# Kernel tuning notes

Measured on AMD Instinct MI355X. Metric: run time of the kernel, lower is better.

The kernel has to match this reference:

```python
import jax, jax.numpy as jnp
import numpy as np


def _apply_1q_batched(state, gate, q):
    # state: (B,2,2,2,2) complex; gate: (B,2,2) complex; acts on qubit q
    state = jnp.moveaxis(state, q + 1, -1)
    state = jnp.einsum('bij,b...j->b...i', gate, state)
    return jnp.moveaxis(state, -1, q + 1)


def _apply_cnot(state, c, t):
    # flip target bit where control bit == 1
    s0, s1 = jnp.split(state, 2, axis=c + 1)
    s1 = jnp.flip(s1, axis=t + 1)
    return jnp.concatenate([s0, s1], axis=c + 1)


def _quantum_features(angles, params):
    # angles: (B,4) RY rotation angles; params: (4,) RZ angles
    B = angles.shape[0]
    state = jnp.zeros((B, 16), jnp.complex64).at[:, 0].set(1.0).reshape(B, 2, 2, 2, 2)
    # RY(x_i) on each wire (batched angle per sample)
    for q in range(4):
        th = 0.5 * angles[:, q]
        c, s = jnp.cos(th), jnp.sin(th)
        gate = jnp.stack([jnp.stack([c, -s], -1), jnp.stack([s, c], -1)], -2).astype(jnp.complex64)
        state = _apply_1q_batched(state, gate, q)
    # RZ(params[i]) on wire i followed by CNOT(i, (i+1)%4), interleaved as in source
    pc = params.astype(jnp.complex64)
    for q in range(4):
        ph = jnp.exp(jnp.array([-0.5j, 0.5j], jnp.complex64) * pc[q])
        shp = [1, 1, 1, 1, 1]
        shp[q + 1] = 2
        state = state * ph.reshape(shp)
        state = _apply_cnot(state, q, (q + 1) % 4)
    probs = state.real ** 2 + state.imag ** 2  # (B,2,2,2,2)
    feats = []
    for q in range(4):
        axes = tuple(a for a in range(1, 5) if a != q + 1)
        p = probs.sum(axes)  # (B,2)
        feats.append(p[:, 0] - p[:, 1])  # <Z_q>
    return jnp.stack(feats, -1)  # (B,4)


def _deconv2x2(x, w, b):
    # PyTorch ConvTranspose2d with kernel=stride=2, padding=0 (non-overlapping)
    # x: (B,Ci,H,W), w: (Ci,Co,2,2), b: (Co,)
    B, Ci, H, W = x.shape
    Co = w.shape[1]
    y = jnp.einsum('bchw,codk->bohdwk', x, w).reshape(B, Co, 2 * H, 2 * W)
    return y + b[None, :, None, None]


def setup_inputs() -> dict:
    key = jax.random.key(0)
    ks = jax.random.split(key, 10)
    B = 16384
    return {
        'x': jax.random.uniform(ks[0], (B, 1, 28, 28), jnp.float32),
        'var_params': jax.random.normal(ks[1], (4,), jnp.float32),
        'w_lat': jax.random.normal(ks[2], (224, 4), jnp.float32) * 0.3,
        'b_lat': jax.random.normal(ks[3], (224,), jnp.float32) * 0.05,
        'w_fc': jax.random.normal(ks[4], (392, 224), jnp.float32) * 0.05,
        'b_fc': jax.random.normal(ks[5], (392,), jnp.float32) * 0.05,
        'w_d1': jax.random.normal(ks[6], (8, 4, 2, 2), jnp.float32) * 0.2,
        'b_d1': jax.random.normal(ks[7], (4,), jnp.float32) * 0.05,
        'w_d2': jax.random.normal(ks[8], (4, 1, 2, 2), jnp.float32) * 0.2,
        'b_d2': jax.random.normal(ks[9], (1,), jnp.float32) * 0.05,
    }


def reference(x, var_params, w_lat, b_lat, w_fc, b_fc, w_d1, b_d1, w_d2, b_d2):
    # quadrant means -> 4 angles per sample
    quad = jnp.stack([
        x[:, 0, :14, :14].mean((1, 2)),
        x[:, 0, :14, 14:].mean((1, 2)),
        x[:, 0, 14:, :14].mean((1, 2)),
        x[:, 0, 14:, 14:].mean((1, 2)),
    ], axis=1)  # (B,4)
    qf = _quantum_features(quad, var_params)  # (B,4)
    latent = jax.nn.relu(qf @ w_lat.T + b_lat)  # (B,224)
    h = jax.nn.relu(latent @ w_fc.T + b_fc)  # (B,392)
    h = h.reshape(-1, 8, 7, 7)
    h = jax.nn.relu(_deconv2x2(h, w_d1, b_d1))  # (B,4,14,14)
    out = jax.nn.sigmoid(_deconv2x2(h, w_d2, b_d2))  # (B,1,28,28)
    return out
```

## Files before the change

kernel.cpp:

```cpp
#include <hip/hip_runtime.h>
#include <math.h>

#define G 16
#define HS 396
#define LSTR 232

typedef __attribute__((ext_vector_type(8))) __bf16 bf16x8;
typedef __attribute__((ext_vector_type(4))) float f32x4;

__global__ void wconv_kernel(const float* __restrict__ w_fc, __bf16* __restrict__ wb) {
  int tile = blockIdx.x;
  int kt   = blockIdx.y;
  int lane = threadIdx.x;
  int n  = tile * 16 + (lane & 15);
  int k0 = kt * 32 + (lane >> 4) * 8;
  bf16x8 v;
  if (n < 392) {
    const float* src = w_fc + (size_t)n * 224 + k0;
    float4 f0 = *(const float4*)(src);
    float4 f1 = *(const float4*)(src + 4);
    v[0] = (__bf16)f0.x; v[1] = (__bf16)f0.y; v[2] = (__bf16)f0.z; v[3] = (__bf16)f0.w;
    v[4] = (__bf16)f1.x; v[5] = (__bf16)f1.y; v[6] = (__bf16)f1.z; v[7] = (__bf16)f1.w;
  } else {
    #pragma unroll
    for (int j = 0; j < 8; ++j) v[j] = (__bf16)0.f;
  }
  *(bf16x8*)(wb + ((size_t)(tile * 7 + kt) * 64 + lane) * 8) = v;
}

__global__ __launch_bounds__(256) void qsum_kernel(
    const float* __restrict__ x, float* __restrict__ angles, int B)
{
  int wave = threadIdx.x >> 6;
  int lane = threadIdx.x & 63;
  int s = blockIdx.x * 4 + wave;
  if (s >= B) return;
  const float4* xs4 = (const float4*)(x + (size_t)s * 784);
  float st0 = 0.f, st1 = 0.f, sb0 = 0.f, sb1 = 0.f;
  for (int i4 = lane; i4 < 196; i4 += 64) {
    float4 v = xs4[i4];
    int base = i4 * 4;
    int r = base / 28;
    int cb = base - r * 28;
    float bt = (r >= 14) ? 1.f : 0.f;
    float tp = 1.f - bt;
    float vals[4] = {v.x, v.y, v.z, v.w};
    #pragma unroll
    for (int e = 0; e < 4; ++e) {
      float val = vals[e];
      bool right = (cb + e) >= 14;
      float l = right ? 0.f : val;
      float rr = right ? val : 0.f;
      st0 = fmaf(tp, l, st0);
      st1 = fmaf(tp, rr, st1);
      sb0 = fmaf(bt, l, sb0);
      sb1 = fmaf(bt, rr, sb1);
    }
  }
  #pragma unroll
  for (int o = 32; o > 0; o >>= 1) {
    st0 += __shfl_down(st0, o, 64);
    st1 += __shfl_down(st1, o, 64);
    sb0 += __shfl_down(sb0, o, 64);
    sb1 += __shfl_down(sb1, o, 64);
  }
  if (lane == 0) {
    const float inv = 1.f / 196.f;
    float4 o;
    o.x = st0 * inv; o.y = st1 * inv; o.z = sb0 * inv; o.w = sb1 * inv;
    *(float4*)(angles + 4 * s) = o;
  }
}

__global__ __launch_bounds__(256) void qsim_kernel(
    const float* __restrict__ params, float* __restrict__ qfa, int B)
{
  int s = blockIdx.x * 256 + threadIdx.x;
  if (s >= B) return;
  float4 mn = *(const float4*)(qfa + 4 * s);
  float means[4] = {mn.x, mn.y, mn.z, mn.w};
  float cs[4], sn[4];
  #pragma unroll
  for (int q = 0; q < 4; ++q) {
    float th = 0.5f * means[q];
    sn[q] = __sinf(th);
    cs[q] = __cosf(th);
  }
  float re[16], im[16];
  #pragma unroll
  for (int idx = 0; idx < 16; ++idx) {
    float a = ((idx >> 3) & 1) ? sn[0] : cs[0];
    a *= ((idx >> 2) & 1) ? sn[1] : cs[1];
    a *= ((idx >> 1) & 1) ? sn[2] : cs[2];
    a *= (idx & 1) ? sn[3] : cs[3];
    re[idx] = a;
    im[idx] = 0.f;
  }
  #pragma unroll
  for (int q = 0; q < 4; ++q) {
    float hp = 0.5f * params[q];
    float sp = __sinf(hp), cp = __cosf(hp);
    int qb = 3 - q;
    #pragma unroll
    for (int idx = 0; idx < 16; ++idx) {
      float sg = ((idx >> qb) & 1) ? sp : -sp;
      float r0 = re[idx], i0 = im[idx];
      re[idx] = r0 * cp - i0 * sg;
      im[idx] = r0 * sg + i0 * cp;
    }
    int cm = 1 << qb;
    int tm = 1 << (3 - ((q + 1) & 3));
    #pragma unroll
    for (int idx = 0; idx < 16; ++idx) {
      if ((idx & cm) && !(idx & tm)) {
        int j = idx | tm;
        float tr = re[idx]; re[idx] = re[j]; re[j] = tr;
        float ti = im[idx]; im[idx] = im[j]; im[j] = ti;
      }
    }
  }
  float z[4];
  #pragma unroll
  for (int q = 0; q < 4; ++q) {
    int qb = 3 - q;
    float acc = 0.f;
    #pragma unroll
    for (int idx = 0; idx < 16; ++idx) {
      float p = re[idx] * re[idx] + im[idx] * im[idx];
      acc += ((idx >> qb) & 1) ? -p : p;
    }
    z[q] = acc;
  }
  float4 o; o.x = z[0]; o.y = z[1]; o.z = z[2]; o.w = z[3];
  *(float4*)(qfa + 4 * s) = o;
}

__global__ __launch_bounds__(256) void decoder_kernel(
    const float* __restrict__ qf, const __bf16* __restrict__ wb,
    const float* __restrict__ w_lat, const float* __restrict__ b_lat,
    const float* __restrict__ b_fc,
    const float* __restrict__ w_d1, const float* __restrict__ b_d1,
    const float* __restrict__ w_d2, const float* __restrict__ b_d2,
    float* __restrict__ out, int B)
{
  __shared__ __align__(16) __bf16 latb[G * LSTR];
  __shared__ __align__(16) float hbuf[G * HS];
  __shared__ float qfs[G * 4];
  __shared__ float wd1[128];
  __shared__ float wd2[16];
  __shared__ float bd1[4];
  const int t = threadIdx.x;
  const int s0g = blockIdx.x * G;

  if (t < 64) qfs[t] = qf[s0g * 4 + t];
  else if (t < 192) wd1[t - 64] = w_d1[t - 64];
  else if (t < 208) wd2[t - 192] = w_d2[t - 192];
  else if (t < 212) bd1[t - 208] = b_d1[t - 208];
  __syncthreads();

  for (int v = t; v < G * 224; v += 256) {
    int s = v / 224;
    int j = v - s * 224;
    float4 w = *(const float4*)(w_lat + j * 4);
    float a = b_lat[j];
    a = fmaf(qfs[s * 4 + 0], w.x, a);
    a = fmaf(qfs[s * 4 + 1], w.y, a);
    a = fmaf(qfs[s * 4 + 2], w.z, a);
    a = fmaf(qfs[s * 4 + 3], w.w, a);
    latb[s * LSTR + j] = (__bf16)fmaxf(a, 0.f);
  }
  __syncthreads();

  {
    const int wv = t >> 6;
    const int lane = t & 63;
    const int m = lane & 15;
    const int kq = lane >> 4;
    const __bf16* arow = latb + m * LSTR + kq * 8;
    for (int tile = wv; tile < 25; tile += 4) {
      f32x4 acc = {0.f, 0.f, 0.f, 0.f};
      const bf16x8* bp = (const bf16x8*)(wb + ((size_t)(tile * 7) * 64 + lane) * 8);
      #pragma unroll
      for (int kt = 0; kt < 7; ++kt) {
        bf16x8 a = *(const bf16x8*)(arow + kt * 32);
        bf16x8 b = bp[kt * 64];
        acc = __builtin_amdgcn_mfma_f32_16x16x32_bf16(a, b, acc, 0, 0, 0);
      }
      int j = tile * 16 + m;
      if (j < 392) {
        float bf = b_fc[j];
        #pragma unroll
        for (int r = 0; r < 4; ++r)
          hbuf[(kq * 4 + r) * HS + j] = fmaxf(acc[r] + bf, 0.f);
      }
    }
  }
  __syncthreads();

  const float bd2v = b_d2[0];
  for (int v = t; v < G * 196; v += 256) {
    int s = v / 196;
    int p = v - s * 196;
    int Y = p / 14;
    int X = p - Y * 14;
    int y = Y >> 1, ey = Y & 1, xx = X >> 1, ex = X & 1;
    const float* hs = hbuf + s * HS + y * 7 + xx;
    float hv[8];
    #pragma unroll
    for (int ci = 0; ci < 8; ++ci) hv[ci] = hs[ci * 49];
    float o1[4];
    #pragma unroll
    for (int co = 0; co < 4; ++co) {
      float a = bd1[co];
      #pragma unroll
      for (int ci = 0; ci < 8; ++ci)
        a = fmaf(hv[ci], wd1[ci * 16 + co * 4 + ey * 2 + ex], a);
      o1[co] = fmaxf(a, 0.f);
    }
    size_t basep = (size_t)(s0g + s) * 784;
    #pragma unroll
    for (int dy = 0; dy < 2; ++dy) {
      float v0 = bd2v, v1 = bd2v;
      #pragma unroll
      for (int co = 0; co < 4; ++co) {
        v0 = fmaf(o1[co], wd2[co * 4 + dy * 2 + 0], v0);
        v1 = fmaf(o1[co], wd2[co * 4 + dy * 2 + 1], v1);
      }
      float2 o;
      o.x = 1.f / (1.f + __expf(-v0));
      o.y = 1.f / (1.f + __expf(-v1));
      *(float2*)(out + basep + (size_t)(2 * Y + dy) * 28 + 2 * X) = o;
    }
  }
}

extern "C" void kernel_launch(void* const* d_in, const int* in_sizes, int n_in,
                              void* d_out, int out_size, void* d_ws, size_t ws_size,
                              hipStream_t stream) {
  const float* x          = (const float*)d_in[0];
  const float* var_params = (const float*)d_in[1];
  const float* w_lat      = (const float*)d_in[2];
  const float* b_lat      = (const float*)d_in[3];
  const float* w_fc       = (const float*)d_in[4];
  const float* b_fc       = (const float*)d_in[5];
  const float* w_d1       = (const float*)d_in[6];
  const float* b_d1       = (const float*)d_in[7];
  const float* w_d2       = (const float*)d_in[8];
  const float* b_d2       = (const float*)d_in[9];
  float* out = (float*)d_out;

  __bf16* wb   = (__bf16*)d_ws;
  float* qfa   = (float*)((char*)d_ws + 262144);

  int B = in_sizes[0] / 784;
  wconv_kernel<<<dim3(25, 7), 64, 0, stream>>>(w_fc, wb);
  qsum_kernel<<<(B + 3) / 4, 256, 0, stream>>>(x, qfa, B);
  qsim_kernel<<<(B + 255) / 256, 256, 0, stream>>>(var_params, qfa, B);
  decoder_kernel<<<(B + G - 1) / G, 256, 0, stream>>>(
      qfa, wb, w_lat, b_lat, b_fc, w_d1, b_d1, w_d2, b_d2, out, B);
}
```

Baseline: 142.8 us.

## Fuse quadrant sums and quantum simulation into the decoder kernel

Merges the quadrant-mean reduction and the 4-qubit simulation into the decoder kernel, so each block reads its 16 input images, computes angles and features in shared memory, then runs the MLP and deconvs. This removes two kernel launches and the global round trip of the angle and feature buffer. It also adds nontemporal loads for x and nontemporal stores for the output, plus a launch-bounds occupancy hint. The risk is less parallelism in the reduction phase and the qsim step running on only 16 threads per block while the rest idle.

```diff
diff --git a/kernel.cpp b/kernel.cpp
--- a/kernel.cpp
+++ b/kernel.cpp
@@ -7,6 +7,7 @@
 
 typedef __attribute__((ext_vector_type(8))) __bf16 bf16x8;
 typedef __attribute__((ext_vector_type(4))) float f32x4;
+typedef __attribute__((ext_vector_type(2))) float f32x2;
 
 __global__ void wconv_kernel(const float* __restrict__ w_fc, __bf16* __restrict__ wb) {
   int tile = blockIdx.x;
@@ -28,115 +29,9 @@
   *(bf16x8*)(wb + ((size_t)(tile * 7 + kt) * 64 + lane) * 8) = v;
 }
 
-__global__ __launch_bounds__(256) void qsum_kernel(
-    const float* __restrict__ x, float* __restrict__ angles, int B)
-{
-  int wave = threadIdx.x >> 6;
-  int lane = threadIdx.x & 63;
-  int s = blockIdx.x * 4 + wave;
-  if (s >= B) return;
-  const float4* xs4 = (const float4*)(x + (size_t)s * 784);
-  float st0 = 0.f, st1 = 0.f, sb0 = 0.f, sb1 = 0.f;
-  for (int i4 = lane; i4 < 196; i4 += 64) {
-    float4 v = xs4[i4];
-    int base = i4 * 4;
-    int r = base / 28;
-    int cb = base - r * 28;
-    float bt = (r >= 14) ? 1.f : 0.f;
-    float tp = 1.f - bt;
-    float vals[4] = {v.x, v.y, v.z, v.w};
-    #pragma unroll
-    for (int e = 0; e < 4; ++e) {
-      float val = vals[e];
-      bool right = (cb + e) >= 14;
-      float l = right ? 0.f : val;
-      float rr = right ? val : 0.f;
-      st0 = fmaf(tp, l, st0);
-      st1 = fmaf(tp, rr, st1);
-      sb0 = fmaf(bt, l, sb0);
-      sb1 = fmaf(bt, rr, sb1);
-    }
-  }
-  #pragma unroll
-  for (int o = 32; o > 0; o >>= 1) {
-    st0 += __shfl_down(st0, o, 64);
-    st1 += __shfl_down(st1, o, 64);
-    sb0 += __shfl_down(sb0, o, 64);
-    sb1 += __shfl_down(sb1, o, 64);
-  }
-  if (lane == 0) {
-    const float inv = 1.f / 196.f;
-    float4 o;
-    o.x = st0 * inv; o.y = st1 * inv; o.z = sb0 * inv; o.w = sb1 * inv;
-    *(float4*)(angles + 4 * s) = o;
-  }
-}
-
-__global__ __launch_bounds__(256) void qsim_kernel(
-    const float* __restrict__ params, float* __restrict__ qfa, int B)
-{
-  int s = blockIdx.x * 256 + threadIdx.x;
-  if (s >= B) return;
-  float4 mn = *(const float4*)(qfa + 4 * s);
-  float means[4] = {mn.x, mn.y, mn.z, mn.w};
-  float cs[4], sn[4];
-  #pragma unroll
-  for (int q = 0; q < 4; ++q) {
-    float th = 0.5f * means[q];
-    sn[q] = __sinf(th);
-    cs[q] = __cosf(th);
-  }
-  float re[16], im[16];
-  #pragma unroll
-  for (int idx = 0; idx < 16; ++idx) {
-    float a = ((idx >> 3) & 1) ? sn[0] : cs[0];
-    a *= ((idx >> 2) & 1) ? sn[1] : cs[1];
-    a *= ((idx >> 1) & 1) ? sn[2] : cs[2];
-    a *= (idx & 1) ? sn[3] : cs[3];
-    re[idx] = a;
-    im[idx] = 0.f;
-  }
-  #pragma unroll
-  for (int q = 0; q < 4; ++q) {
-    float hp = 0.5f * params[q];
-    float sp = __sinf(hp), cp = __cosf(hp);
-    int qb = 3 - q;
-    #pragma unroll
-    for (int idx = 0; idx < 16; ++idx) {
-      float sg = ((idx >> qb) & 1) ? sp : -sp;
-      float r0 = re[idx], i0 = im[idx];
-      re[idx] = r0 * cp - i0 * sg;
-      im[idx] = r0 * sg + i0 * cp;
-    }
-    int cm = 1 << qb;
-    int tm = 1 << (3 - ((q + 1) & 3));
-    #pragma unroll
-    for (int idx = 0; idx < 16; ++idx) {
-      if ((idx & cm) && !(idx & tm)) {
-        int j = idx | tm;
-        float tr = re[idx]; re[idx] = re[j]; re[j] = tr;
-        float ti = im[idx]; im[idx] = im[j]; im[j] = ti;
-      }
-    }
-  }
-  float z[4];
-  #pragma unroll
-  for (int q = 0; q < 4; ++q) {
-    int qb = 3 - q;
-    float acc = 0.f;
-    #pragma unroll
-    for (int idx = 0; idx < 16; ++idx) {
-      float p = re[idx] * re[idx] + im[idx] * im[idx];
-      acc += ((idx >> qb) & 1) ? -p : p;
-    }
-    z[q] = acc;
-  }
-  float4 o; o.x = z[0]; o.y = z[1]; o.z = z[2]; o.w = z[3];
-  *(float4*)(qfa + 4 * s) = o;
-}
-
-__global__ __launch_bounds__(256) void decoder_kernel(
-    const float* __restrict__ qf, const __bf16* __restrict__ wb,
+__global__ __launch_bounds__(256, 4) void fused_kernel(
+    const float* __restrict__ x, const float* __restrict__ params,
+    const __bf16* __restrict__ wb,
     const float* __restrict__ w_lat, const float* __restrict__ b_lat,
     const float* __restrict__ b_fc,
     const float* __restrict__ w_d1, const float* __restrict__ b_d1,
@@ -150,12 +45,121 @@
   __shared__ float wd2[16];
   __shared__ float bd1[4];
   const int t = threadIdx.x;
+  const int wv = t >> 6;
+  const int lane = t & 63;
   const int s0g = blockIdx.x * G;
-
-  if (t < 64) qfs[t] = qf[s0g * 4 + t];
-  else if (t < 192) wd1[t - 64] = w_d1[t - 64];
-  else if (t < 208) wd2[t - 192] = w_d2[t - 192];
-  else if (t < 212) bd1[t - 208] = b_d1[t - 208];
+  if (s0g >= B) return;
+
+  if (t < 128) wd1[t] = w_d1[t];
+  else if (t < 144) wd2[t - 128] = w_d2[t - 128];
+  else if (t < 148) bd1[t - 144] = b_d1[t - 144];
+
+  {
+    const float* xb = x + (size_t)(s0g + wv * 4) * 784;
+    float acc[4][4];
+    #pragma unroll
+    for (int i = 0; i < 4; ++i)
+      #pragma unroll
+      for (int q = 0; q < 4; ++q) acc[i][q] = 0.f;
+    for (int i4 = lane; i4 < 196; i4 += 64) {
+      int base = i4 * 4;
+      int r = base / 28;
+      int cb = base - r * 28;
+      float bt = (r >= 14) ? 1.f : 0.f;
+      float tp = 1.f - bt;
+      float w0[4], w1[4], w2[4], w3[4];
+      #pragma unroll
+      for (int e = 0; e < 4; ++e) {
+        float lf = ((cb + e) < 14) ? 1.f : 0.f;
+        float rf = 1.f - lf;
+        w0[e] = tp * lf; w1[e] = tp * rf; w2[e] = bt * lf; w3[e] = bt * rf;
+      }
+      #pragma unroll
+      for (int smp = 0; smp < 4; ++smp) {
+        f32x4 v = __builtin_nontemporal_load((const f32x4*)(xb + smp * 784 + base));
+        #pragma unroll
+        for (int e = 0; e < 4; ++e) {
+          acc[smp][0] = fmaf(v[e], w0[e], acc[smp][0]);
+          acc[smp][1] = fmaf(v[e], w1[e], acc[smp][1]);
+          acc[smp][2] = fmaf(v[e], w2[e], acc[smp][2]);
+          acc[smp][3] = fmaf(v[e], w3[e], acc[smp][3]);
+        }
+      }
+    }
+    #pragma unroll
+    for (int smp = 0; smp < 4; ++smp)
+      #pragma unroll
+      for (int q = 0; q < 4; ++q)
+        #pragma unroll
+        for (int o = 32; o > 0; o >>= 1)
+          acc[smp][q] += __shfl_down(acc[smp][q], o, 64);
+    if (lane == 0) {
+      const float inv = 1.f / 196.f;
+      #pragma unroll
+      for (int smp = 0; smp < 4; ++smp) {
+        float4 o;
+        o.x = acc[smp][0] * inv; o.y = acc[smp][1] * inv;
+        o.z = acc[smp][2] * inv; o.w = acc[smp][3] * inv;
+        *(float4*)(qfs + (wv * 4 + smp) * 4) = o;
+      }
+    }
+  }
+  __syncthreads();
+
+  if (t < G) {
+    float means[4] = {qfs[t * 4], qfs[t * 4 + 1], qfs[t * 4 + 2], qfs[t * 4 + 3]};
+    float cs[4], sn[4];
+    #pragma unroll
+    for (int q = 0; q < 4; ++q) {
+      float th = 0.5f * means[q];
+      sn[q] = __sinf(th);
+      cs[q] = __cosf(th);
+    }
+    float re[16], im[16];
+    #pragma unroll
+    for (int idx = 0; idx < 16; ++idx) {
+      float a = ((idx >> 3) & 1) ? sn[0] : cs[0];
+      a *= ((idx >> 2) & 1) ? sn[1] : cs[1];
+      a *= ((idx >> 1) & 1) ? sn[2] : cs[2];
+      a *= (idx & 1) ? sn[3] : cs[3];
+      re[idx] = a;
+      im[idx] = 0.f;
+    }
+    #pragma unroll
+    for (int q = 0; q < 4; ++q) {
+      float hp = 0.5f * params[q];
+      float sp = __sinf(hp), cp = __cosf(hp);
+      int qb = 3 - q;
+      #pragma unroll
+      for (int idx = 0; idx < 16; ++idx) {
+        float sg = ((idx >> qb) & 1) ? sp : -sp;
+        float r0 = re[idx], i0 = im[idx];
+        re[idx] = r0 * cp - i0 * sg;
+        im[idx] = r0 * sg + i0 * cp;
+      }
+      int cm = 1 << qb;
+      int tm = 1 << (3 - ((q + 1) & 3));
+      #pragma unroll
+      for (int idx = 0; idx < 16; ++idx) {
+        if ((idx & cm) && !(idx & tm)) {
+          int j = idx | tm;
+          float tr = re[idx]; re[idx] = re[j]; re[j] = tr;
+          float ti = im[idx]; im[idx] = im[j]; im[j] = ti;
+        }
+      }
+    }
+    #pragma unroll
+    for (int q = 0; q < 4; ++q) {
+      int qb = 3 - q;
+      float z = 0.f;
+      #pragma unroll
+      for (int idx = 0; idx < 16; ++idx) {
+        float p = re[idx] * re[idx] + im[idx] * im[idx];
+        z += ((idx >> qb) & 1) ? -p : p;
+      }
+      qfs[t * 4 + q] = z;
+    }
+  }
   __syncthreads();
 
   for (int v = t; v < G * 224; v += 256) {
@@ -172,8 +176,6 @@
   __syncthreads();
 
   {
-    const int wv = t >> 6;
-    const int lane = t & 63;
     const int m = lane & 15;
     const int kq = lane >> 4;
     const __bf16* arow = latb + m * LSTR + kq * 8;
@@ -226,10 +228,10 @@
         v0 = fmaf(o1[co], wd2[co * 4 + dy * 2 + 0], v0);
         v1 = fmaf(o1[co], wd2[co * 4 + dy * 2 + 1], v1);
       }
-      float2 o;
-      o.x = 1.f / (1.f + __expf(-v0));
-      o.y = 1.f / (1.f + __expf(-v1));
-      *(float2*)(out + basep + (size_t)(2 * Y + dy) * 28 + 2 * X) = o;
+      f32x2 o;
+      o[0] = 1.f / (1.f + __expf(-v0));
+      o[1] = 1.f / (1.f + __expf(-v1));
+      __builtin_nontemporal_store(o, (f32x2*)(out + basep + (size_t)(2 * Y + dy) * 28 + 2 * X));
     }
   }
 }
@@ -249,13 +251,10 @@
   const float* b_d2       = (const float*)d_in[9];
   float* out = (float*)d_out;
 
-  __bf16* wb   = (__bf16*)d_ws;
-  float* qfa   = (float*)((char*)d_ws + 262144);
+  __bf16* wb = (__bf16*)d_ws;
 
   int B = in_sizes[0] / 784;
   wconv_kernel<<<dim3(25, 7), 64, 0, stream>>>(w_fc, wb);
-  qsum_kernel<<<(B + 3) / 4, 256, 0, stream>>>(x, qfa, B);
-  qsim_kernel<<<(B + 255) / 256, 256, 0, stream>>>(var_params, qfa, B);
-  decoder_kernel<<<(B + G - 1) / G, 256, 0, stream>>>(
-      qfa, wb, w_lat, b_lat, b_fc, w_d1, b_d1, w_d2, b_d2, out, B);
+  fused_kernel<<<(B + G - 1) / G, 256, 0, stream>>>(
+      x, var_params, wb, w_lat, b_lat, b_fc, w_d1, b_d1, w_d2, b_d2, out, B);
 }
```

Result: no change. 143.9 us (+0.8%).
